# Kernel optimization log

Hardware: AMD Instinct MI355X
Metric: run time of the kernel (lower is better)

The kernel has to match this reference:

```python
import jax, jax.numpy as jnp
import numpy as np

C, N, B = 16, 65536, 4096  # cases, points per case, batch of case IDs


def _w(key, fan_in, fan_out):
    return jax.random.normal(key, (fan_in, fan_out), dtype=jnp.float32) / np.sqrt(fan_in).astype(np.float32)


def setup_inputs() -> dict:
    key = jax.random.key(0)
    ks = jax.random.split(key, 8)
    pts = jax.random.normal(ks[0], (C, N, 3), dtype=jnp.float32)
    inp = {
        "pts": pts,
        "W1_0": _w(ks[1], 3, 64), "b1_0": jnp.zeros((64,), jnp.float32),
        "W1_1": _w(ks[2], 64, 128), "b1_1": jnp.zeros((128,), jnp.float32),
        "W1_2": _w(ks[3], 128, 512), "b1_2": jnp.zeros((512,), jnp.float32),
        "W2_0": _w(ks[4], 512, 256), "b2_0": jnp.zeros((256,), jnp.float32),
        "W2_1": _w(ks[5], 256, 512), "b2_1": jnp.zeros((512,), jnp.float32),
        "x": jax.random.randint(ks[6], (B,), 0, C, dtype=jnp.int64),
    }
    return inp


def reference(pts, W1_0, b1_0, W1_1, b1_1, W1_2, b1_2, W2_0, b2_0, W2_1, b2_1, x):
    def mlp1(h):  # shared per-point MLP, SiLU after every layer
        h = jax.nn.silu(h @ W1_0 + b1_0)
        h = jax.nn.silu(h @ W1_1 + b1_1)
        h = jax.nn.silu(h @ W1_2 + b1_2)
        return h

    feats = mlp1(pts)                       # [C, N, F1]
    idx = jnp.argmax(feats, axis=1)         # [C, F1] critical-point indices per feature
    # gather critical points (detached in the torch original)
    fixed = jax.lax.stop_gradient(pts[jnp.arange(pts.shape[0])[:, None], idx])  # [C, F1, 3]

    feats2 = mlp1(fixed)                    # [C, F1, F1]
    latent0 = jnp.max(feats2, axis=1)       # [C, F1]

    h = jax.nn.silu(latent0 @ W2_0 + b2_0)  # [C, 256]
    latent = h @ W2_1 + b2_1                # [C, total_modes*ge_features]

    caseID_unit = jax.nn.one_hot(x, latent.shape[0], dtype=latent.dtype)  # [B, C]
    return caseID_unit @ latent             # [B, 512]
```

## Files before the change

### kernel.cpp

```cpp
#include <hip/hip_runtime.h>
#include <math.h>

#define NCASES   16
#define NPTS_BIG 65536
#define F1       512
#define OUT_B    4096

typedef __attribute__((ext_vector_type(8))) short  short8;
typedef __attribute__((ext_vector_type(4))) float  floatx4;

__device__ __forceinline__ float silu_f(float x) {
    return x * __builtin_amdgcn_rcpf(1.0f + __expf(-x));
}

__device__ __forceinline__ unsigned f2bf_hi(float x) {
    unsigned u = __float_as_uint(x);
    return u + 0x7FFFu + ((u >> 16) & 1u);
}
__device__ __forceinline__ unsigned short f2bf(float x) {
    return (unsigned short)(f2bf_hi(x) >> 16);
}
__device__ __forceinline__ unsigned pk2bf_rtz(float lo, float hi) {
    return __builtin_amdgcn_perm(__float_as_uint(hi), __float_as_uint(lo), 0x07060302u);
}

__device__ __forceinline__ unsigned enc_f(float x) {
    unsigned u = __float_as_uint(x);
    return (u & 0x80000000u) ? ~u : (u | 0x80000000u);
}
__device__ __forceinline__ float dec_f(unsigned e) {
    unsigned u = (e & 0x80000000u) ? (e ^ 0x80000000u) : ~e;
    return __uint_as_float(u);
}

__device__ __forceinline__ float sgpr_f(float x) {
    return __uint_as_float(__builtin_amdgcn_readfirstlane(__float_as_uint(x)));
}

__global__ void k_prep(const float* __restrict__ W11, const float* __restrict__ W12,
                       unsigned short* __restrict__ BbWs, unsigned short* __restrict__ BcWs,
                       unsigned long long* __restrict__ argBufs)
{
    int i = blockIdx.x * 256 + threadIdx.x;
    if (i < 16384) argBufs[i] = 0ull;
    {
        int j = i & 7, l = (i >> 3) & 63, t = i >> 9;
        int KT = t & 3, NT = (t >> 2) & 3, w = t >> 4;
        int k = KT * 32 + (l >> 4) * 8 + j;
        int f = w * 64 + NT * 16 + (l & 15);
        BcWs[i] = f2bf(W12[(size_t)k * 512 + f]);
    }
    if (i < 8192) {
        int j = i & 7, l = (i >> 3) & 63, t = i >> 9;
        int KT = t & 1, w = t >> 1;
        int k = KT * 32 + (l >> 4) * 8 + j;
        int f = w * 16 + (l & 15);
        BbWs[i] = f2bf(W11[(size_t)k * 128 + f]);
    }
}

template<bool GATHER>
__global__ __launch_bounds__(512, 4)
void k_mlp1_argmax(const float* __restrict__ pts, int nPts, int chunksPerBlock,
                   const unsigned long long* __restrict__ gatherIdx,
                   const float* __restrict__ W10, const float* __restrict__ b10,
                   const float* __restrict__ b11, const float* __restrict__ b12,
                   const unsigned short* __restrict__ BbWs,
                   const unsigned short* __restrict__ BcWs,
                   unsigned long long* __restrict__ argOut)
{
    const int c   = blockIdx.y;
    const int tid = threadIdx.x;
    const int w   = tid >> 6;
    const int l   = tid & 63;
    const int lm  = l & 15;
    const int q   = l >> 4;

    __shared__ __align__(16) unsigned short s_h0[64][72];
    __shared__ __align__(16) unsigned short s_h1[64][136];

    const int wf = __builtin_amdgcn_readfirstlane(w);

    float wA0[8], wA1[8], wA2[8], bA[8];
    #pragma unroll
    for (int j = 0; j < 8; ++j) {
        wA0[j] = sgpr_f(W10[  0 + wf * 8 + j]);
        wA1[j] = sgpr_f(W10[ 64 + wf * 8 + j]);
        wA2[j] = sgpr_f(W10[128 + wf * 8 + j]);
        bA[j]  = sgpr_f(b10[       wf * 8 + j]);
    }

    short8 Bc[16];
    #pragma unroll
    for (int t = 0; t < 16; ++t)
        Bc[t] = *(const short8*)(BcWs + (size_t)((wf * 16 + t) * 64 + l) * 8);
    short8 Bb[2];
    #pragma unroll
    for (int t = 0; t < 2; ++t)
        Bb[t] = *(const short8*)(BbWs + (size_t)((wf * 2 + t) * 64 + l) * 8);

    const float bias11 = b11[wf * 16 + lm];

    float bestv[4];
    #pragma unroll
    for (int NT = 0; NT < 4; ++NT) bestv[NT] = -INFINITY;

    const float* cpts = pts + (size_t)c * nPts * 3;

    for (int ch = 0; ch < chunksPerBlock; ++ch) {
        const int pbase = (blockIdx.x * chunksPerBlock + ch) * 64;

        {
            float x, y, z;
            if (GATHER) {
                unsigned gi = ~(unsigned)(gatherIdx[(size_t)c * 512 + pbase + l] & 0xFFFFFFFFull);
                const float* sp = cpts + (size_t)gi * 3;
                x = sp[0]; y = sp[1]; z = sp[2];
            } else {
                const float* sp = cpts + (size_t)(pbase + l) * 3;
                x = sp[0]; y = sp[1]; z = sp[2];
            }
            float v[8];
            #pragma unroll
            for (int j = 0; j < 8; ++j) {
                float t = fmaf(z, wA2[j], bA[j]);
                t = fmaf(y, wA1[j], t);
                t = fmaf(x, wA0[j], t);
                v[j] = silu_f(t);
            }
            uint4 hv = { pk2bf_rtz(v[0], v[1]), pk2bf_rtz(v[2], v[3]),
                         pk2bf_rtz(v[4], v[5]), pk2bf_rtz(v[6], v[7]) };
            *(uint4*)&s_h0[l][wf * 8] = hv;
        }
        __syncthreads();

        #pragma unroll
        for (int MT = 0; MT < 4; ++MT) {
            short8 a0 = *(const short8*)&s_h0[MT * 16 + lm][q * 8];
            short8 a1 = *(const short8*)&s_h0[MT * 16 + lm][32 + q * 8];
            floatx4 acc = {bias11, bias11, bias11, bias11};
            acc = __builtin_amdgcn_mfma_f32_16x16x32_bf16(a0, Bb[0], acc, 0, 0, 0);
            acc = __builtin_amdgcn_mfma_f32_16x16x32_bf16(a1, Bb[1], acc, 0, 0, 0);
            #pragma unroll
            for (int r = 0; r < 4; ++r) {
                unsigned uv = __float_as_uint(silu_f(acc[r]));
                s_h1[MT * 16 + q * 4 + r][wf * 16 + lm] = (unsigned short)(uv >> 16);
            }
        }
        __syncthreads();

        const int cb0 = 127 - (ch << 4);
        #pragma unroll
        for (int MT = 0; MT < 4; ++MT) {
            short8 a[4];
            #pragma unroll
            for (int KT = 0; KT < 4; ++KT)
                a[KT] = *(const short8*)&s_h1[MT * 16 + lm][KT * 32 + q * 8];
            const int cbM = cb0 - (MT << 2);
            #pragma unroll
            for (int NT = 0; NT < 4; ++NT) {
                floatx4 acc = {0.f, 0.f, 0.f, 0.f};
                #pragma unroll
                for (int KT = 0; KT < 4; ++KT)
                    acc = __builtin_amdgcn_mfma_f32_16x16x32_bf16(a[KT], Bc[NT * 4 + KT], acc, 0, 0, 0);
                float x0 = __uint_as_float((__float_as_uint(acc[0]) & 0xFFFFFF80u) | (unsigned)(cbM));
                float x1 = __uint_as_float((__float_as_uint(acc[1]) & 0xFFFFFF80u) | (unsigned)(cbM - 1));
                float x2 = __uint_as_float((__float_as_uint(acc[2]) & 0xFFFFFF80u) | (unsigned)(cbM - 2));
                float x3 = __uint_as_float((__float_as_uint(acc[3]) & 0xFFFFFF80u) | (unsigned)(cbM - 3));
                float t0 = fmaxf(fmaxf(x0, x1), x2);
                bestv[NT] = fmaxf(fmaxf(t0, x3), bestv[NT]);
            }
        }
    }

    #pragma unroll
    for (int NT = 0; NT < 4; ++NT) {
        unsigned u = __float_as_uint(bestv[NT]);
        int t = 127 - (int)(u & 127u);
        unsigned idx = (unsigned)((blockIdx.x * chunksPerBlock + (t >> 4)) * 64
                                  + ((t >> 2) & 3) * 16 + q * 4 + (t & 3));
        float v = __uint_as_float(u & 0xFFFFFF80u) + b12[wf * 64 + NT * 16 + lm];
        #pragma unroll
        for (int m = 16; m <= 32; m <<= 1) {
            float    vo = __shfl_xor(v, m, 64);
            unsigned io = __shfl_xor(idx, m, 64);
            if (vo > v || (vo == v && io < idx)) { v = vo; idx = io; }
        }
        if (q == 0) {
            unsigned long long key = ((unsigned long long)enc_f(v) << 32)
                                   | (unsigned long long)(~idx);
            atomicMax(&argOut[(size_t)c * 512 + wf * 64 + NT * 16 + lm], key);
        }
    }
}

__global__ __launch_bounds__(256)
void k_head(const unsigned long long* __restrict__ argBuf2,
            const float* __restrict__ W20, const float* __restrict__ b20,
            const float* __restrict__ W21, const float* __restrict__ b21,
            float* __restrict__ latent)
{
    const int c = blockIdx.x, tid = threadIdx.x;
    __shared__ float l0[512];
    __shared__ float hh[256];
    l0[tid]       = silu_f(dec_f((unsigned)(argBuf2[(size_t)c * 512 + tid] >> 32)));
    l0[tid + 256] = silu_f(dec_f((unsigned)(argBuf2[(size_t)c * 512 + tid + 256] >> 32)));
    __syncthreads();
    float acc = b20[tid];
    for (int k = 0; k < 512; ++k) acc += l0[k] * W20[(size_t)k * 256 + tid];
    hh[tid] = silu_f(acc);
    __syncthreads();
    #pragma unroll
    for (int r = 0; r < 2; ++r) {
        int f = tid + r * 256;
        float a2 = b21[f];
        for (int k = 0; k < 256; ++k) a2 += hh[k] * W21[(size_t)k * 512 + f];
        latent[(size_t)c * 512 + f] = a2;
    }
}

__global__ void k_scatter(const int* __restrict__ x,
                          const float* __restrict__ latent,
                          float* __restrict__ out)
{
    const int b = blockIdx.x, t = threadIdx.x;
    int cid = x[b];
    const float4* src = (const float4*)(latent + (size_t)cid * 512);
    float4* dst = (float4*)(out + (size_t)b * 512);
    dst[t] = src[t];
}

extern "C" void kernel_launch(void* const* d_in, const int* in_sizes, int n_in,
                              void* d_out, int out_size, void* d_ws, size_t ws_size,
                              hipStream_t stream)
{
    const float* pts = (const float*)d_in[0];
    const float* W10 = (const float*)d_in[1];
    const float* b10 = (const float*)d_in[2];
    const float* W11 = (const float*)d_in[3];
    const float* b11 = (const float*)d_in[4];
    const float* W12 = (const float*)d_in[5];
    const float* b12 = (const float*)d_in[6];
    const float* W20 = (const float*)d_in[7];
    const float* b20 = (const float*)d_in[8];
    const float* W21 = (const float*)d_in[9];
    const float* b21 = (const float*)d_in[10];
    const int*   x   = (const int*)d_in[11];
    float* out = (float*)d_out;

    char* ws = (char*)d_ws;
    unsigned long long* argBuf  = (unsigned long long*)ws;
    unsigned long long* argBuf2 = (unsigned long long*)(ws + 65536);
    float* latent               = (float*)(ws + 131072);
    unsigned short* BbWs        = (unsigned short*)(ws + 163840);
    unsigned short* BcWs        = (unsigned short*)(ws + 180224);

    k_prep<<<dim3(256), dim3(256), 0, stream>>>(W11, W12, BbWs, BcWs, argBuf);

    k_mlp1_argmax<false><<<dim3(128, NCASES), dim3(512), 0, stream>>>(
        pts, NPTS_BIG, 8, nullptr, W10, b10, b11, b12, BbWs, BcWs, argBuf);

    k_mlp1_argmax<true><<<dim3(8, NCASES), dim3(512), 0, stream>>>(
        pts, NPTS_BIG, 1, argBuf, W10, b10, b11, b12, BbWs, BcWs, argBuf2);

    k_head<<<dim3(NCASES), dim3(256), 0, stream>>>(argBuf2, W20, b20, W21, b21, latent);

    k_scatter<<<dim3(OUT_B), dim3(128), 0, stream>>>(x, latent, out);
}
```

Before: 264.5 us.

## Double chunk size to 128 points and prefetch next chunk's point coordinates

Each loop iteration now processes 128 points instead of 64, halving the number of barriers per point and the chunk count per block. The coordinates for the next chunk are loaded right after the first barrier so the global load latency overlaps with the MFMA work of the current chunk. The index encoding in the low bits is adjusted to the new chunk geometry. The cost is twice the shared memory per block and more live registers, which may lower occupancy under the 512-thread, 4-blocks launch bound.

```diff
diff --git a/kernel.cpp b/kernel.cpp
--- a/kernel.cpp
+++ b/kernel.cpp
@@ -76,8 +76,8 @@
     const int lm  = l & 15;
     const int q   = l >> 4;
 
-    __shared__ __align__(16) unsigned short s_h0[64][72];
-    __shared__ __align__(16) unsigned short s_h1[64][136];
+    __shared__ __align__(16) unsigned short s_h0[128][72];
+    __shared__ __align__(16) unsigned short s_h1[128][136];
 
     const int wf = __builtin_amdgcn_readfirstlane(w);
 
@@ -100,6 +100,8 @@
         Bb[t] = *(const short8*)(BbWs + (size_t)((wf * 2 + t) * 64 + l) * 8);
 
     const float bias11 = b11[wf * 16 + lm];
+    const floatx4 fzero = {0.f, 0.f, 0.f, 0.f};
+    const floatx4 bias4 = {bias11, bias11, bias11, bias11};
 
     float bestv[4];
     #pragma unroll
@@ -107,39 +109,59 @@
 
     const float* cpts = pts + (size_t)c * nPts * 3;
 
+    float ax[2], ay[2], az[2];
+    {
+        const int pb = blockIdx.x * chunksPerBlock * 128;
+        #pragma unroll
+        for (int h = 0; h < 2; ++h) {
+            const float* sp;
+            if (GATHER) {
+                unsigned gi = ~(unsigned)(gatherIdx[(size_t)c * 512 + pb + h * 64 + l] & 0xFFFFFFFFull);
+                sp = cpts + (size_t)gi * 3;
+            } else {
+                sp = cpts + (size_t)(pb + h * 64 + l) * 3;
+            }
+            ax[h] = sp[0]; ay[h] = sp[1]; az[h] = sp[2];
+        }
+    }
+
     for (int ch = 0; ch < chunksPerBlock; ++ch) {
-        const int pbase = (blockIdx.x * chunksPerBlock + ch) * 64;
-
-        {
-            float x, y, z;
-            if (GATHER) {
-                unsigned gi = ~(unsigned)(gatherIdx[(size_t)c * 512 + pbase + l] & 0xFFFFFFFFull);
-                const float* sp = cpts + (size_t)gi * 3;
-                x = sp[0]; y = sp[1]; z = sp[2];
-            } else {
-                const float* sp = cpts + (size_t)(pbase + l) * 3;
-                x = sp[0]; y = sp[1]; z = sp[2];
-            }
+        #pragma unroll
+        for (int h = 0; h < 2; ++h) {
             float v[8];
             #pragma unroll
             for (int j = 0; j < 8; ++j) {
-                float t = fmaf(z, wA2[j], bA[j]);
-                t = fmaf(y, wA1[j], t);
-                t = fmaf(x, wA0[j], t);
+                float t = fmaf(az[h], wA2[j], bA[j]);
+                t = fmaf(ay[h], wA1[j], t);
+                t = fmaf(ax[h], wA0[j], t);
                 v[j] = silu_f(t);
             }
             uint4 hv = { pk2bf_rtz(v[0], v[1]), pk2bf_rtz(v[2], v[3]),
                          pk2bf_rtz(v[4], v[5]), pk2bf_rtz(v[6], v[7]) };
-            *(uint4*)&s_h0[l][wf * 8] = hv;
+            *(uint4*)&s_h0[h * 64 + l][wf * 8] = hv;
         }
         __syncthreads();
 
-        #pragma unroll
-        for (int MT = 0; MT < 4; ++MT) {
+        if (ch + 1 < chunksPerBlock) {
+            const int pb = (blockIdx.x * chunksPerBlock + ch + 1) * 128;
+            #pragma unroll
+            for (int h = 0; h < 2; ++h) {
+                const float* sp;
+                if (GATHER) {
+                    unsigned gi = ~(unsigned)(gatherIdx[(size_t)c * 512 + pb + h * 64 + l] & 0xFFFFFFFFull);
+                    sp = cpts + (size_t)gi * 3;
+                } else {
+                    sp = cpts + (size_t)(pb + h * 64 + l) * 3;
+                }
+                ax[h] = sp[0]; ay[h] = sp[1]; az[h] = sp[2];
+            }
+        }
+
+        #pragma unroll
+        for (int MT = 0; MT < 8; ++MT) {
             short8 a0 = *(const short8*)&s_h0[MT * 16 + lm][q * 8];
             short8 a1 = *(const short8*)&s_h0[MT * 16 + lm][32 + q * 8];
-            floatx4 acc = {bias11, bias11, bias11, bias11};
-            acc = __builtin_amdgcn_mfma_f32_16x16x32_bf16(a0, Bb[0], acc, 0, 0, 0);
+            floatx4 acc = __builtin_amdgcn_mfma_f32_16x16x32_bf16(a0, Bb[0], bias4, 0, 0, 0);
             acc = __builtin_amdgcn_mfma_f32_16x16x32_bf16(a1, Bb[1], acc, 0, 0, 0);
             #pragma unroll
             for (int r = 0; r < 4; ++r) {
@@ -149,19 +171,18 @@
         }
         __syncthreads();
 
-        const int cb0 = 127 - (ch << 4);
-        #pragma unroll
-        for (int MT = 0; MT < 4; ++MT) {
+        #pragma unroll
+        for (int MT = 0; MT < 8; ++MT) {
             short8 a[4];
             #pragma unroll
             for (int KT = 0; KT < 4; ++KT)
                 a[KT] = *(const short8*)&s_h1[MT * 16 + lm][KT * 32 + q * 8];
-            const int cbM = cb0 - (MT << 2);
+            const int cbM = 127 - (ch << 5) - (MT << 2);
             #pragma unroll
             for (int NT = 0; NT < 4; ++NT) {
-                floatx4 acc = {0.f, 0.f, 0.f, 0.f};
+                floatx4 acc = __builtin_amdgcn_mfma_f32_16x16x32_bf16(a[0], Bc[NT * 4], fzero, 0, 0, 0);
                 #pragma unroll
-                for (int KT = 0; KT < 4; ++KT)
+                for (int KT = 1; KT < 4; ++KT)
                     acc = __builtin_amdgcn_mfma_f32_16x16x32_bf16(a[KT], Bc[NT * 4 + KT], acc, 0, 0, 0);
                 float x0 = __uint_as_float((__float_as_uint(acc[0]) & 0xFFFFFF80u) | (unsigned)(cbM));
                 float x1 = __uint_as_float((__float_as_uint(acc[1]) & 0xFFFFFF80u) | (unsigned)(cbM - 1));
@@ -177,8 +198,8 @@
     for (int NT = 0; NT < 4; ++NT) {
         unsigned u = __float_as_uint(bestv[NT]);
         int t = 127 - (int)(u & 127u);
-        unsigned idx = (unsigned)((blockIdx.x * chunksPerBlock + (t >> 4)) * 64
-                                  + ((t >> 2) & 3) * 16 + q * 4 + (t & 3));
+        unsigned idx = (unsigned)((blockIdx.x * chunksPerBlock + (t >> 5)) * 128
+                                  + ((t >> 2) & 7) * 16 + q * 4 + (t & 3));
         float v = __uint_as_float(u & 0xFFFFFF80u) + b12[wf * 64 + NT * 16 + lm];
         #pragma unroll
         for (int m = 16; m <= 32; m <<= 1) {
@@ -258,9 +279,9 @@
     k_prep<<<dim3(256), dim3(256), 0, stream>>>(W11, W12, BbWs, BcWs, argBuf);
 
     k_mlp1_argmax<false><<<dim3(128, NCASES), dim3(512), 0, stream>>>(
-        pts, NPTS_BIG, 8, nullptr, W10, b10, b11, b12, BbWs, BcWs, argBuf);
-
-    k_mlp1_argmax<true><<<dim3(8, NCASES), dim3(512), 0, stream>>>(
+        pts, NPTS_BIG, 4, nullptr, W10, b10, b11, b12, BbWs, BcWs, argBuf);
+
+    k_mlp1_argmax<true><<<dim3(4, NCASES), dim3(512), 0, stream>>>(
         pts, NPTS_BIG, 1, argBuf, W10, b10, b11, b12, BbWs, BcWs, argBuf2);
 
     k_head<<<dim3(NCASES), dim3(256), 0, stream>>>(argBuf2, W20, b20, W21, b21, latent);
```

New measurement: 267.3 us. Within noise of the previous version (+1.0%).
